# Performance work log

Hardware: AMD Instinct MI355X
Metric: run time of the kernel (lower is better)

Reference implementation:

```python
import jax, jax.numpy as jnp
import numpy as np

B, L, D, H = 2, 2048, 1024, 16
HD = D // H


def _xavier(key, out_f, in_f):
    std = (2.0 / (in_f + out_f)) ** 0.5
    return jax.random.normal(key, (out_f, in_f), dtype=jnp.float32) * std


def setup_inputs() -> dict:
    key = jax.random.key(0)
    k = jax.random.split(key, 8)
    Q = jax.random.normal(k[0], (B, L, D), dtype=jnp.float32)
    K = jax.random.normal(k[1], (B, L, D), dtype=jnp.float32)
    V = jax.random.normal(k[2], (B, L, D), dtype=jnp.float32)
    mask = jnp.tril(jnp.ones((L, L), dtype=jnp.int32))[None, None]  # causal [1,1,L,L]
    wq = _xavier(k[3], D, D)
    wk = _xavier(k[4], D, D)
    wv = _xavier(k[5], D, D)
    wo = _xavier(k[6], D, D)
    bo = jnp.zeros((D,), dtype=jnp.float32)
    return {"Q": Q, "K": K, "V": V, "mask": mask,
            "wq": wq, "wk": wk, "wv": wv, "wo": wo, "bo": bo}


def reference(Q, K, V, mask, wq, wk, wv, wo, bo):
    N, Lq, Dm = Q.shape
    # projections: X @ W^T (Linear stores [out, in])
    q = (Q @ wq.T).reshape(N, Lq, H, HD).transpose(0, 2, 1, 3)  # [N,H,L,hd]
    kk = (K @ wk.T).reshape(N, Lq, H, HD).transpose(0, 2, 1, 3)
    v = (V @ wv.T).reshape(N, Lq, H, HD).transpose(0, 2, 1, 3)
    score = jnp.einsum('bhqd,bhkd->bhqk', q, kk) / jnp.sqrt(jnp.float32(HD))
    score = jnp.where(mask == 0, -jnp.inf, score)
    weights = jax.nn.softmax(score, axis=-1)
    attn = jnp.einsum('bhqk,bhkd->bhqd', weights, v)
    out = attn.transpose(0, 2, 1, 3).reshape(N, Lq, Dm)
    return out @ wo.T + bo
```

## Files before the change

### kernel.cpp

```cpp
#include <hip/hip_runtime.h>
#include <hip/hip_bf16.h>


#define B_ 2
#define L_ 2048
#define D_ 1024
#define H_ 16
#define HD_ 64

typedef __attribute__((ext_vector_type(8))) short bf16x8;
typedef __attribute__((ext_vector_type(4))) float f32x4;
typedef __hip_bfloat16 bf16;

__device__ __forceinline__ void async_load16(const void* g, void* l) {
  __builtin_amdgcn_global_load_lds((const __attribute__((address_space(1))) void*)g,
                                   (__attribute__((address_space(3))) void*)l,
                                   16, 0, 0);
}

__global__ __launch_bounds__(256) void wcvt_kernel(const float* __restrict__ w0,
                                                   const float* __restrict__ w1,
                                                   const float* __restrict__ w2,
                                                   const float* __restrict__ w3,
                                                   bf16* __restrict__ dst) {
  const int z = blockIdx.y;
  const float* src = (z == 0) ? w0 : (z == 1) ? w1 : (z == 2) ? w2 : w3;
  int i = (blockIdx.x * 256 + threadIdx.x) * 4;
  float4 v = *(const float4*)(src + i);
  union { bf16 h[4]; uint2 u; } pk;
  pk.h[0] = __float2bfloat16(v.x);
  pk.h[1] = __float2bfloat16(v.y);
  pk.h[2] = __float2bfloat16(v.z);
  pk.h[3] = __float2bfloat16(v.w);
  *(uint2*)(dst + (size_t)z * D_ * D_ + i) = pk.u;
}

__device__ __forceinline__ bf16x8 a_frag_f32(const float* As, int row, int quad) {
  const int sw = row & 7;
  f32x4 a = *(const f32x4*)&As[row * 32 + (((2 * quad) ^ sw) * 4)];
  f32x4 b = *(const f32x4*)&As[row * 32 + (((2 * quad + 1) ^ sw) * 4)];
  union { bf16 h[8]; bf16x8 v; } u;
  u.h[0] = __float2bfloat16(a[0]);
  u.h[1] = __float2bfloat16(a[1]);
  u.h[2] = __float2bfloat16(a[2]);
  u.h[3] = __float2bfloat16(a[3]);
  u.h[4] = __float2bfloat16(b[0]);
  u.h[5] = __float2bfloat16(b[1]);
  u.h[6] = __float2bfloat16(b[2]);
  u.h[7] = __float2bfloat16(b[3]);
  return u.v;
}

__global__ __launch_bounds__(256) void gemm_qkv(const float* __restrict__ Qf,
                                                const float* __restrict__ Kf,
                                                const float* __restrict__ Vf,
                                                const bf16* __restrict__ Wb,
                                                bf16* __restrict__ qp,
                                                bf16* __restrict__ kp,
                                                bf16* __restrict__ vtp) {
  __shared__ __align__(16) float Asf[128 * 32];
  __shared__ __align__(16) bf16 Bs[128 * 32];
  const int tid = threadIdx.x;
  const int wv = tid >> 6, lane = tid & 63;
  const int quad = lane >> 4, l16 = lane & 15;
  const int wm = wv & 1, wn = wv >> 1;
  const int m0 = blockIdx.x * 128, n0 = blockIdx.y * 128;
  const int z = blockIdx.z;
  const float* X = (z == 0) ? Qf : (z == 1) ? Kf : Vf;
  const bf16* W = Wb + (size_t)z * D_ * D_;

  f32x4 acc[4][4];
#pragma unroll
  for (int i = 0; i < 4; i++)
#pragma unroll
    for (int j = 0; j < 4; j++) acc[i][j] = (f32x4){0.f, 0.f, 0.f, 0.f};

  for (int k0 = 0; k0 < D_; k0 += 32) {
#pragma unroll
    for (int it = 0; it < 4; it++) {
      int s = it * 256 + tid;
      int r = s >> 3, c = (s & 7) ^ (r & 7);
      async_load16(X + (size_t)(m0 + r) * D_ + k0 + c * 4, (char*)Asf + s * 16);
    }
#pragma unroll
    for (int it = 0; it < 2; it++) {
      int c = (wv * 2 + it) * 64 + lane;
      int row = c >> 2, cc = c & 3;
      async_load16(W + (size_t)(n0 + row) * D_ + k0 + cc * 8, (char*)Bs + c * 16);
    }
    __syncthreads();
    bf16x8 af[4], bfr[4];
#pragma unroll
    for (int mi = 0; mi < 4; mi++)
      af[mi] = a_frag_f32(Asf, wm * 64 + mi * 16 + l16, quad);
#pragma unroll
    for (int ni = 0; ni < 4; ni++)
      bfr[ni] = *(const bf16x8*)&Bs[(wn * 64 + ni * 16 + l16) * 32 + quad * 8];
#pragma unroll
    for (int mi = 0; mi < 4; mi++)
#pragma unroll
      for (int ni = 0; ni < 4; ni++)
        acc[mi][ni] = __builtin_amdgcn_mfma_f32_16x16x32_bf16(af[mi], bfr[ni],
                                                              acc[mi][ni], 0, 0, 0);
    __syncthreads();
  }

  const float sc = (z == 0) ? 0.125f : 1.0f;
#pragma unroll
  for (int mi = 0; mi < 4; mi++) {
#pragma unroll
    for (int ni = 0; ni < 4; ni++) {
      int n = n0 + wn * 64 + ni * 16 + l16;
#pragma unroll
      for (int r = 0; r < 4; r++) {
        int m = m0 + wm * 64 + mi * 16 + quad * 4 + r;
        bf16 v = __float2bfloat16(acc[mi][ni][r] * sc);
        if (z == 2) {
          int b = m >> 11, l = m & (L_ - 1);
          int h = n >> 6, hd = n & 63;
          vtp[((size_t)((b * H_ + h) * HD_ + hd)) * L_ + l] = v;
        } else {
          ((z == 0) ? qp : kp)[(size_t)m * D_ + n] = v;
        }
      }
    }
  }
}

__global__ __launch_bounds__(256) void attn_kernel(const bf16* __restrict__ qp,
                                                   const bf16* __restrict__ kp,
                                                   const bf16* __restrict__ vt,
                                                   bf16* __restrict__ attn) {
  __shared__ __align__(16) bf16 Kt[2][64 * 64];
  __shared__ __align__(16) bf16 Vt[2][64 * 64];
  __shared__ __align__(16) bf16 Pl[4][16 * 72];
  __shared__ __align__(16) bf16 Ph[4][16 * 72];
  const int tid = threadIdx.x;
  const int wv = tid >> 6, lane = tid & 63;
  const int quad = lane >> 4, l16 = lane & 15;
  const int pair = blockIdx.x, h = blockIdx.y, b = blockIdx.z;
  const int qlo = pair, qhi = (L_ / 64 - 1) - pair;

  const int rL = qlo * 64 + wv * 16 + l16;
  const int rH = qhi * 64 + wv * 16 + l16;
  bf16x8 qaL[2], qaH[2];
#pragma unroll
  for (int kk = 0; kk < 2; kk++) {
    qaL[kk] = *(const bf16x8*)&qp[((size_t)(b * L_ + rL)) * D_ + h * HD_ +
                                  kk * 32 + quad * 8];
    qaH[kk] = *(const bf16x8*)&qp[((size_t)(b * L_ + rH)) * D_ + h * HD_ +
                                  kk * 32 + quad * 8];
  }

  f32x4 OL[4], OH[4];
#pragma unroll
  for (int t = 0; t < 4; t++) {
    OL[t] = (f32x4){0.f, 0.f, 0.f, 0.f};
    OH[t] = (f32x4){0.f, 0.f, 0.f, 0.f};
  }
  float lL[4] = {0.f, 0.f, 0.f, 0.f}, lH[4] = {0.f, 0.f, 0.f, 0.f};

  const int csw = quad ^ (l16 & 7);

  auto stage = [&](int j, int buf) {
    const int j0 = j * 64;
#pragma unroll
    for (int it = 0; it < 2; it++) {
      int slot = (wv * 2 + it) * 64 + lane;
      int row = slot >> 3, c = (slot & 7) ^ (row & 7);
      async_load16(kp + ((size_t)(b * L_ + j0 + row)) * D_ + h * HD_ + c * 8,
                   (char*)Kt[buf] + slot * 16);
      async_load16(vt + ((size_t)((b * H_ + h) * HD_ + row)) * L_ + j0 + c * 8,
                   (char*)Vt[buf] + slot * 16);
    }
  };

  stage(0, 0);
  for (int j = 0; j <= qhi; j++) {
    const int buf = j & 1;
    const int j0 = j * 64;
    const bool doLo = (j <= qlo);
    __syncthreads();
    if (j < qhi) stage(j + 1, buf ^ 1);

    f32x4 sL[4], sH[4];
#pragma unroll
    for (int ss = 0; ss < 4; ss++) {
      int krow = ss * 16 + l16;
      bf16x8 kb0 = *(const bf16x8*)&Kt[buf][krow * 64 + csw * 8];
      bf16x8 kb1 = *(const bf16x8*)&Kt[buf][krow * 64 + (csw ^ 4) * 8];
      f32x4 s = (f32x4){0.f, 0.f, 0.f, 0.f};
      s = __builtin_amdgcn_mfma_f32_16x16x32_bf16(qaH[0], kb0, s, 0, 0, 0);
      s = __builtin_amdgcn_mfma_f32_16x16x32_bf16(qaH[1], kb1, s, 0, 0, 0);
      sH[ss] = s;
      if (doLo) {
        f32x4 t = (f32x4){0.f, 0.f, 0.f, 0.f};
        t = __builtin_amdgcn_mfma_f32_16x16x32_bf16(qaL[0], kb0, t, 0, 0, 0);
        t = __builtin_amdgcn_mfma_f32_16x16x32_bf16(qaL[1], kb1, t, 0, 0, 0);
        sL[ss] = t;
      }
    }

    if (j == qhi) {
#pragma unroll
      for (int ss = 0; ss < 4; ss++) {
        int key = j0 + ss * 16 + l16;
#pragma unroll
        for (int r = 0; r < 4; r++) {
          int rq = qhi * 64 + wv * 16 + quad * 4 + r;
          if (key > rq) sH[ss][r] = -1e30f;
        }
      }
    }
    if (doLo && j == qlo) {
#pragma unroll
      for (int ss = 0; ss < 4; ss++) {
        int key = j0 + ss * 16 + l16;
#pragma unroll
        for (int r = 0; r < 4; r++) {
          int rq = qlo * 64 + wv * 16 + quad * 4 + r;
          if (key > rq) sL[ss][r] = -1e30f;
        }
      }
    }
#pragma unroll
    for (int ss = 0; ss < 4; ss++) {
#pragma unroll
      for (int r = 0; r < 4; r++) {
        float p = __expf(sH[ss][r]);
        lH[r] += p;
        Ph[wv][(quad * 4 + r) * 72 + ss * 16 + l16] = __float2bfloat16(p);
      }
    }
    if (doLo) {
#pragma unroll
      for (int ss = 0; ss < 4; ss++) {
#pragma unroll
        for (int r = 0; r < 4; r++) {
          float p = __expf(sL[ss][r]);
          lL[r] += p;
          Pl[wv][(quad * 4 + r) * 72 + ss * 16 + l16] = __float2bfloat16(p);
        }
      }
    }

    asm volatile("s_waitcnt lgkmcnt(0)" ::: "memory");

#pragma unroll
    for (int kk = 0; kk < 2; kk++) {
      bf16x8 pah = *(const bf16x8*)&Ph[wv][l16 * 72 + kk * 32 + quad * 8];
      bf16x8 pal;
      if (doLo) pal = *(const bf16x8*)&Pl[wv][l16 * 72 + kk * 32 + quad * 8];
#pragma unroll
      for (int t = 0; t < 4; t++) {
        bf16x8 vb = *(const bf16x8*)&Vt[buf][(t * 16 + l16) * 64 + (csw ^ (kk * 4)) * 8];
        OH[t] = __builtin_amdgcn_mfma_f32_16x16x32_bf16(pah, vb, OH[t], 0, 0, 0);
        if (doLo) OL[t] = __builtin_amdgcn_mfma_f32_16x16x32_bf16(pal, vb, OL[t], 0, 0, 0);
      }
    }
  }

#pragma unroll
  for (int r = 0; r < 4; r++) {
#pragma unroll
    for (int off = 1; off < 16; off <<= 1) {
      lL[r] += __shfl_xor(lL[r], off, 64);
      lH[r] += __shfl_xor(lH[r], off, 64);
    }
  }
#pragma unroll
  for (int t = 0; t < 4; t++) {
#pragma unroll
    for (int r = 0; r < 4; r++) {
      int rowL = qlo * 64 + wv * 16 + quad * 4 + r;
      int rowH = qhi * 64 + wv * 16 + quad * 4 + r;
      attn[((size_t)(b * L_ + rowL)) * D_ + h * HD_ + t * 16 + l16] =
          __float2bfloat16(OL[t][r] / lL[r]);
      attn[((size_t)(b * L_ + rowH)) * D_ + h * HD_ + t * 16 + l16] =
          __float2bfloat16(OH[t][r] / lH[r]);
    }
  }
}

__global__ __launch_bounds__(256) void gemm_out(const bf16* __restrict__ X,
                                                const bf16* __restrict__ W,
                                                const float* __restrict__ bias,
                                                float* __restrict__ out) {
  __shared__ __align__(16) bf16 As[64 * 32];
  __shared__ __align__(16) bf16 Bs[128 * 32];
  const int tid = threadIdx.x;
  const int wv = tid >> 6, lane = tid & 63;
  const int quad = lane >> 4, l16 = lane & 15;
  const int wm = wv & 1, wn = wv >> 1;
  const int m0 = blockIdx.x * 64, n0 = blockIdx.y * 128;

  f32x4 acc[2][4];
#pragma unroll
  for (int i = 0; i < 2; i++)
#pragma unroll
    for (int j = 0; j < 4; j++) acc[i][j] = (f32x4){0.f, 0.f, 0.f, 0.f};

  for (int k0 = 0; k0 < D_; k0 += 32) {
    {
      int c = tid;
      int row = c >> 2, cc = c & 3;
      async_load16(X + (size_t)(m0 + row) * D_ + k0 + cc * 8, (char*)As + c * 16);
    }
#pragma unroll
    for (int it = 0; it < 2; it++) {
      int c = (wv * 2 + it) * 64 + lane;
      int row = c >> 2, cc = c & 3;
      async_load16(W + (size_t)(n0 + row) * D_ + k0 + cc * 8, (char*)Bs + c * 16);
    }
    __syncthreads();
    bf16x8 af[2], bfr[4];
#pragma unroll
    for (int mi = 0; mi < 2; mi++)
      af[mi] = *(const bf16x8*)&As[(wm * 32 + mi * 16 + l16) * 32 + quad * 8];
#pragma unroll
    for (int ni = 0; ni < 4; ni++)
      bfr[ni] = *(const bf16x8*)&Bs[(wn * 64 + ni * 16 + l16) * 32 + quad * 8];
#pragma unroll
    for (int mi = 0; mi < 2; mi++)
#pragma unroll
      for (int ni = 0; ni < 4; ni++)
        acc[mi][ni] = __builtin_amdgcn_mfma_f32_16x16x32_bf16(af[mi], bfr[ni],
                                                              acc[mi][ni], 0, 0, 0);
    __syncthreads();
  }

#pragma unroll
  for (int mi = 0; mi < 2; mi++) {
#pragma unroll
    for (int ni = 0; ni < 4; ni++) {
      int n = n0 + wn * 64 + ni * 16 + l16;
      float bval = bias[n];
#pragma unroll
      for (int r = 0; r < 4; r++) {
        int m = m0 + wm * 32 + mi * 16 + quad * 4 + r;
        out[(size_t)m * D_ + n] = acc[mi][ni][r] + bval;
      }
    }
  }
}

extern "C" void kernel_launch(void* const* d_in, const int* in_sizes, int n_in,
                              void* d_out, int out_size, void* d_ws, size_t ws_size,
                              hipStream_t stream) {
  const float* Q  = (const float*)d_in[0];
  const float* K  = (const float*)d_in[1];
  const float* V  = (const float*)d_in[2];
  const float* wq = (const float*)d_in[4];
  const float* wk = (const float*)d_in[5];
  const float* wvp = (const float*)d_in[6];
  const float* wo = (const float*)d_in[7];
  const float* bo = (const float*)d_in[8];
  float* out = (float*)d_out;

  const size_t NA = (size_t)B_ * L_ * D_;
  const size_t NW = (size_t)D_ * D_;
  bf16* Wb = (bf16*)d_ws;
  bf16* qp = Wb + 4 * NW;
  bf16* kp = qp + NA;
  bf16* vt = kp + NA;
  bf16* at = vt + NA;

  wcvt_kernel<<<dim3(NW / 1024, 4), 256, 0, stream>>>(wq, wk, wvp, wo, Wb);
  gemm_qkv<<<dim3(32, 8, 3), 256, 0, stream>>>(Q, K, V, Wb, qp, kp, vt);
  attn_kernel<<<dim3(L_ / 128, H_, B_), 256, 0, stream>>>(qp, kp, vt, at);
  gemm_out<<<dim3(64, 8), 256, 0, stream>>>(at, Wb + 3 * NW, bo, out);
}
```

Before: 252.9 us.

## Double-buffer LDS tiles and XOR-swizzle bf16 rows in projection GEMMs

Both the QKV projection and output projection GEMMs now use two LDS buffers. The next K-tile's async global-to-LDS loads are issued right after a single barrier, so they overlap the MFMA work on the current tile, and the trailing barrier is removed. The bf16 tiles also get an XOR swizzle on their 16-byte chunks, keyed per row, to cut LDS bank conflicts on fragment reads. In exchange, LDS use per block doubles, which may reduce occupancy, and the code relies on the barrier to wait for outstanding async loads.

```diff
diff --git a/kernel.cpp b/kernel.cpp
--- a/kernel.cpp
+++ b/kernel.cpp
@@ -17,6 +17,8 @@
                                    (__attribute__((address_space(3))) void*)l,
                                    16, 0, 0);
 }
+
+__device__ __forceinline__ int swm(int row) { return (row ^ (row >> 2)) & 3; }
 
 __global__ __launch_bounds__(256) void wcvt_kernel(const float* __restrict__ w0,
                                                    const float* __restrict__ w1,
@@ -58,8 +60,8 @@
                                                 bf16* __restrict__ qp,
                                                 bf16* __restrict__ kp,
                                                 bf16* __restrict__ vtp) {
-  __shared__ __align__(16) float Asf[128 * 32];
-  __shared__ __align__(16) bf16 Bs[128 * 32];
+  __shared__ __align__(16) float Asf[2][128 * 32];
+  __shared__ __align__(16) bf16 Bs[2][128 * 32];
   const int tid = threadIdx.x;
   const int wv = tid >> 6, lane = tid & 63;
   const int quad = lane >> 4, l16 = lane & 15;
@@ -75,34 +77,44 @@
 #pragma unroll
     for (int j = 0; j < 4; j++) acc[i][j] = (f32x4){0.f, 0.f, 0.f, 0.f};
 
-  for (int k0 = 0; k0 < D_; k0 += 32) {
+  auto stage = [&](int k0, int buf) {
 #pragma unroll
     for (int it = 0; it < 4; it++) {
       int s = it * 256 + tid;
       int r = s >> 3, c = (s & 7) ^ (r & 7);
-      async_load16(X + (size_t)(m0 + r) * D_ + k0 + c * 4, (char*)Asf + s * 16);
+      async_load16(X + (size_t)(m0 + r) * D_ + k0 + c * 4,
+                   (char*)Asf[buf] + s * 16);
     }
 #pragma unroll
     for (int it = 0; it < 2; it++) {
       int c = (wv * 2 + it) * 64 + lane;
-      int row = c >> 2, cc = c & 3;
-      async_load16(W + (size_t)(n0 + row) * D_ + k0 + cc * 8, (char*)Bs + c * 16);
-    }
+      int row = c >> 2, cc = (c & 3) ^ swm(row);
+      async_load16(W + (size_t)(n0 + row) * D_ + k0 + cc * 8,
+                   (char*)Bs[buf] + c * 16);
+    }
+  };
+
+  stage(0, 0);
+  for (int k0 = 0; k0 < D_; k0 += 32) {
+    const int buf = (k0 >> 5) & 1;
     __syncthreads();
+    if (k0 + 32 < D_) stage(k0 + 32, buf ^ 1);
+
     bf16x8 af[4], bfr[4];
 #pragma unroll
     for (int mi = 0; mi < 4; mi++)
-      af[mi] = a_frag_f32(Asf, wm * 64 + mi * 16 + l16, quad);
-#pragma unroll
-    for (int ni = 0; ni < 4; ni++)
-      bfr[ni] = *(const bf16x8*)&Bs[(wn * 64 + ni * 16 + l16) * 32 + quad * 8];
+      af[mi] = a_frag_f32(Asf[buf], wm * 64 + mi * 16 + l16, quad);
+#pragma unroll
+    for (int ni = 0; ni < 4; ni++) {
+      int row = wn * 64 + ni * 16 + l16;
+      bfr[ni] = *(const bf16x8*)&Bs[buf][row * 32 + (quad ^ swm(row)) * 8];
+    }
 #pragma unroll
     for (int mi = 0; mi < 4; mi++)
 #pragma unroll
       for (int ni = 0; ni < 4; ni++)
         acc[mi][ni] = __builtin_amdgcn_mfma_f32_16x16x32_bf16(af[mi], bfr[ni],
                                                               acc[mi][ni], 0, 0, 0);
-    __syncthreads();
   }
 
   const float sc = (z == 0) ? 0.125f : 1.0f;
@@ -286,8 +298,8 @@
                                                 const bf16* __restrict__ W,
                                                 const float* __restrict__ bias,
                                                 float* __restrict__ out) {
-  __shared__ __align__(16) bf16 As[64 * 32];
-  __shared__ __align__(16) bf16 Bs[128 * 32];
+  __shared__ __align__(16) bf16 As[2][64 * 32];
+  __shared__ __align__(16) bf16 Bs[2][128 * 32];
   const int tid = threadIdx.x;
   const int wv = tid >> 6, lane = tid & 63;
   const int quad = lane >> 4, l16 = lane & 15;
@@ -300,33 +312,45 @@
 #pragma unroll
     for (int j = 0; j < 4; j++) acc[i][j] = (f32x4){0.f, 0.f, 0.f, 0.f};
 
-  for (int k0 = 0; k0 < D_; k0 += 32) {
+  auto stage = [&](int k0, int buf) {
     {
       int c = tid;
-      int row = c >> 2, cc = c & 3;
-      async_load16(X + (size_t)(m0 + row) * D_ + k0 + cc * 8, (char*)As + c * 16);
+      int row = c >> 2, cc = (c & 3) ^ swm(row);
+      async_load16(X + (size_t)(m0 + row) * D_ + k0 + cc * 8,
+                   (char*)As[buf] + c * 16);
     }
 #pragma unroll
     for (int it = 0; it < 2; it++) {
       int c = (wv * 2 + it) * 64 + lane;
-      int row = c >> 2, cc = c & 3;
-      async_load16(W + (size_t)(n0 + row) * D_ + k0 + cc * 8, (char*)Bs + c * 16);
-    }
+      int row = c >> 2, cc = (c & 3) ^ swm(row);
+      async_load16(W + (size_t)(n0 + row) * D_ + k0 + cc * 8,
+                   (char*)Bs[buf] + c * 16);
+    }
+  };
+
+  stage(0, 0);
+  for (int k0 = 0; k0 < D_; k0 += 32) {
+    const int buf = (k0 >> 5) & 1;
     __syncthreads();
+    if (k0 + 32 < D_) stage(k0 + 32, buf ^ 1);
+
     bf16x8 af[2], bfr[4];
 #pragma unroll
-    for (int mi = 0; mi < 2; mi++)
-      af[mi] = *(const bf16x8*)&As[(wm * 32 + mi * 16 + l16) * 32 + quad * 8];
-#pragma unroll
-    for (int ni = 0; ni < 4; ni++)
-      bfr[ni] = *(const bf16x8*)&Bs[(wn * 64 + ni * 16 + l16) * 32 + quad * 8];
+    for (int mi = 0; mi < 2; mi++) {
+      int row = wm * 32 + mi * 16 + l16;
+      af[mi] = *(const bf16x8*)&As[buf][row * 32 + (quad ^ swm(row)) * 8];
+    }
+#pragma unroll
+    for (int ni = 0; ni < 4; ni++) {
+      int row = wn * 64 + ni * 16 + l16;
+      bfr[ni] = *(const bf16x8*)&Bs[buf][row * 32 + (quad ^ swm(row)) * 8];
+    }
 #pragma unroll
     for (int mi = 0; mi < 2; mi++)
 #pragma unroll
       for (int ni = 0; ni < 4; ni++)
         acc[mi][ni] = __builtin_amdgcn_mfma_f32_16x16x32_bf16(af[mi], bfr[ni],
                                                               acc[mi][ni], 0, 0, 0);
-    __syncthreads();
   }
 
 #pragma unroll
```

Measured after the change: 251.6 us. About the same (-0.5%).
